# Performance work log

Hardware: AMD Instinct MI355X
Metric: run time of the kernel (lower is better)

## Reference

```python
import jax, jax.numpy as jnp
import numpy as np

B, S, D, V = 2, 4096, 2048, 32000
H, HD = 16, 128          # heads, head dim (H*HD == D)
BS = 16                  # block_size
N_ANCH = 128             # num_anchors (static: loss_mask=ones guarantees enough valid positions)
MASK_ID = 31999
DFF = 8192


def rms(x, w, eps=1e-6):
    return x * jax.lax.rsqrt(jnp.mean(x * x, axis=-1, keepdims=True) + eps) * w


def rope(x, pos):
    # x: (..., L, H, hd), pos: (..., L)
    hd = x.shape[-1]
    inv = 1.0 / (10000.0 ** (jnp.arange(0, hd, 2, dtype=jnp.float32) / hd))
    ang = pos[..., None, None].astype(jnp.float32) * inv  # (..., L, 1, hd/2)
    cos, sin = jnp.cos(ang), jnp.sin(ang)
    x1, x2 = x[..., : hd // 2], x[..., hd // 2 :]
    return jnp.concatenate([x1 * cos - x2 * sin, x2 * cos + x1 * sin], axis=-1).astype(x.dtype)


def setup_inputs() -> dict:
    key = jax.random.key(0)
    ks = jax.random.split(key, 12)
    s = 0.02
    return {
        "input_ids": jax.random.randint(ks[0], (B, S), 0, V, dtype=jnp.int32),
        "hidden_states": jax.random.normal(ks[1], (B, S, D), dtype=jnp.float32),
        "loss_mask": jnp.ones((B, S), dtype=jnp.float32),
        "rand_vals": jax.random.uniform(ks[2], (B, S - BS + 1), dtype=jnp.float32),
        "embed_table": jax.random.normal(ks[3], (V, D), dtype=jnp.float32) * s,
        "lm_head_w": jax.random.normal(ks[4], (V, D), dtype=jnp.float32) * s,
        "wq": jax.random.normal(ks[5], (D, D), dtype=jnp.float32) * s,
        "wk": jax.random.normal(ks[6], (D, D), dtype=jnp.float32) * s,
        "wv": jax.random.normal(ks[7], (D, D), dtype=jnp.float32) * s,
        "wo": jax.random.normal(ks[8], (D, D), dtype=jnp.float32) * s,
        "w_gate": jax.random.normal(ks[9], (D, DFF), dtype=jnp.float32) * s,
        "w_up": jax.random.normal(ks[10], (D, DFF), dtype=jnp.float32) * s,
        "w_down": jax.random.normal(ks[11], (DFF, D), dtype=jnp.float32) * s,
        "norm_attn": jnp.ones((D,), dtype=jnp.float32),
        "norm_mlp": jnp.ones((D,), dtype=jnp.float32),
        "norm_out": jnp.ones((D,), dtype=jnp.float32),
        "norm_chs": jnp.ones((D,), dtype=jnp.float32),
    }


def reference(input_ids, hidden_states, loss_mask, rand_vals, embed_table, lm_head_w,
              wq, wk, wv, wo, w_gate, w_up, w_down, norm_attn, norm_mlp, norm_out, norm_chs):
    max_anchor = S - BS
    # ---- anchor sampling: random permutation of valid positions via argsort of rand ----
    valid = loss_mask[:, : max_anchor + 1] > 0.5                       # (B, max_anchor+1)
    valid_counts = valid.sum(axis=1)
    idx = jnp.arange(max_anchor + 1, dtype=jnp.int32)
    masked_idx = jnp.where(valid, idx[None, :], S + 1)
    rv = jnp.where(valid, rand_vals, 2.0)
    order = jnp.argsort(rv, axis=1)
    gathered = jnp.take_along_axis(masked_idx, order, axis=1)
    anchors = jnp.sort(gathered[:, :N_ANCH], axis=1)                   # (B, N)
    keep = jnp.arange(N_ANCH)[None, :] < jnp.minimum(valid_counts, N_ANCH)[:, None]
    anchors = jnp.where(keep, anchors, 0)
    # ---- noise embedding: anchor token at block start, mask token elsewhere ----
    anchor_tok = jnp.take_along_axis(input_ids, jnp.clip(anchors, 0, S - 1), axis=1)
    first_tok = jnp.where(keep, anchor_tok, MASK_ID)
    noise_ids = jnp.full((B, N_ANCH, BS), MASK_ID, dtype=jnp.int32).at[:, :, 0].set(first_tok)
    x = embed_table[noise_ids]                                         # (B,N,BS,D)
    # ---- CHS context hidden: target hidden at anchor-1 ----
    ctx_pos = jnp.maximum(anchors - 1, 0)
    ctx = jnp.take_along_axis(hidden_states, ctx_pos[:, :, None], axis=1)  # (B,N,D)
    # ---- block-diagonal attention: per-block kv = [CHS_i | draft block i] (kv_len=1+BS) ----
    pos_q = anchors[:, :, None] + jnp.arange(BS)[None, None, :]        # (B,N,BS)
    pos_kv = jnp.concatenate([ctx_pos[:, :, None], pos_q], axis=2)     # (B,N,1+BS)
    hq = rms(x, norm_attn)
    hc = rms(ctx, norm_chs)[:, :, None, :]
    kv_in = jnp.concatenate([hc, hq], axis=2)                          # (B,N,1+BS,D)
    q = rope((hq @ wq).reshape(B, N_ANCH, BS, H, HD), pos_q)
    k = rope((kv_in @ wk).reshape(B, N_ANCH, 1 + BS, H, HD), pos_kv)
    v = (kv_in @ wv).reshape(B, N_ANCH, 1 + BS, H, HD)
    scores = jnp.einsum('bnqhd,bnkhd->bnhqk', q, k) * (1.0 / HD ** 0.5)
    attn = jax.nn.softmax(scores, axis=-1)
    out = jnp.einsum('bnhqk,bnkhd->bnqhd', attn, v).reshape(B, N_ANCH, BS, D) @ wo
    out = out * keep[:, :, None, None].astype(out.dtype)               # invalid blocks fully masked
    x = x + out
    h = rms(x, norm_mlp)
    x = x + (jax.nn.silu(h @ w_gate) * (h @ w_up)) @ w_down
    h_out = rms(x, norm_out)
    logits = h_out @ lm_head_w.T                                       # (B,N,BS,V)
    # ---- block-wise CE loss ----
    label_idx = anchors[:, :, None] + jnp.arange(BS)[None, None, :]
    valid_label = label_idx < S
    safe = jnp.minimum(label_idx, S - 1)
    targets = jnp.take_along_axis(jnp.broadcast_to(input_ids[:, None, :], (B, N_ANCH, S)), safe, axis=2)
    lm_g = jnp.take_along_axis(jnp.broadcast_to(loss_mask[:, None, :], (B, N_ANCH, S)), safe, axis=2)
    weight = (keep[:, :, None] & valid_label).astype(jnp.float32)
    weight = weight * (jnp.arange(BS) > 0)[None, None, :].astype(jnp.float32) * lm_g
    logp = jax.nn.log_softmax(logits, axis=-1)
    tok_logp = jnp.take_along_axis(logp, targets[..., None].astype(jnp.int32), axis=-1)[..., 0]
    loss = -(tok_logp * weight).sum() / (weight.sum() + 1e-6)
    pred = jnp.argmax(logits, axis=-1)
    accuracy = ((pred == targets) & (weight > 0.5)).sum().astype(jnp.float32) / (weight.sum() + 1e-6)
    return loss, accuracy
```

## Files before the change

### kernel.cpp

```cpp
#include <hip/hip_runtime.h>
#include <math.h>

typedef unsigned short u16;
typedef short v8s __attribute__((ext_vector_type(8)));
typedef u16   v4u __attribute__((ext_vector_type(4)));
typedef float v4f __attribute__((ext_vector_type(4)));

#define DEVFN static __device__ __forceinline__

constexpr int cB = 2, cS = 4096, cD = 2048, cV = 32000, cH = 16, cHD = 128;
constexpr int cBS = 16, cNA = 128, cMASK = 31999, cDFF = 8192;
constexpr int NCAND = cS - cBS + 1;
constexpr int MTOK  = cB * cNA * cBS;
constexpr int MKV   = cB * cNA * 17;
constexpr int NCH   = cV / 128;
constexpr int NCH2  = cV / 256;

constexpr int EPI_BF16 = 0, EPI_SILU = 1, EPI_OEMB = 2, EPI_DOWNACC = 3, EPI_STATS = 4;
constexpr int ASRC_BF16 = 0, ASRC_RMS = 1, ASRC_AOMAP = 2;

struct RmsSrc {
  const float* hs; const float* emb; const float* nattn; const float* nchs;
  const float* rowinv; const int* ftok; const int* cpos;
};

DEVFN u16 f2bf(float f) {
  union { float f; unsigned u; } a; a.f = f;
  unsigned u = a.u;
  u = u + 0x7fffu + ((u >> 16) & 1u);
  return (u16)(u >> 16);
}
DEVFN float bf2f(u16 h) {
  union { unsigned u; float f; } a; a.u = ((unsigned)h) << 16;
  return a.f;
}
DEVFN float waveSum(float v) {
  #pragma unroll
  for (int o = 32; o >= 1; o >>= 1) v += __shfl_xor(v, o);
  return v;
}
DEVFN void gload16(void* lds, const void* g) {
  __builtin_amdgcn_global_load_lds(
      (const __attribute__((address_space(1))) unsigned*)g,
      (__attribute__((address_space(3))) unsigned*)lds, 16, 0, 0);
}

__global__ void k_select(const float* __restrict__ lmask, const float* __restrict__ rv_in,
                         int* __restrict__ self) {
  int b = blockIdx.x >> 4, chunk = blockIdx.x & 15;
  __shared__ float rvs[4096];
  for (int i = threadIdx.x; i < NCAND; i += 256) {
    bool valid = lmask[(size_t)b * cS + i] > 0.5f;
    rvs[i] = valid ? rv_in[(size_t)b * NCAND + i] : 2.0f;
  }
  __syncthreads();
  int i = chunk * 256 + threadIdx.x;
  if (i < NCAND) {
    float v = rvs[i];
    int rank = 0;
    for (int j = 0; j < NCAND; ++j) {
      float u = rvs[j];
      rank += (u < v) || (u == v && j < i);
    }
    self[(size_t)b * NCAND + i] = (rank < cNA) ? 1 : 0;
  }
}

__global__ void k_anchors(const float* __restrict__ lmask, const int* __restrict__ self,
                          const int* __restrict__ ids, int* __restrict__ anchors,
                          int* __restrict__ keepA, int* __restrict__ ftok, int* __restrict__ cpos) {
  int b = blockIdx.x;
  __shared__ int flags[4096];
  __shared__ int ssum[256];
  __shared__ int soff[257];
  __shared__ int abuf[cNA];
  for (int i = threadIdx.x; i < 4096; i += 256)
    flags[i] = (i < NCAND) ? (self[(size_t)b * NCAND + i] && (lmask[(size_t)b * cS + i] > 0.5f)) : 0;
  if (threadIdx.x < cNA) abuf[threadIdx.x] = 0;
  __syncthreads();
  int s = 0;
  #pragma unroll
  for (int j = 0; j < 16; ++j) s += flags[threadIdx.x * 16 + j];
  ssum[threadIdx.x] = s;
  __syncthreads();
  if (threadIdx.x == 0) {
    int a = 0;
    for (int t = 0; t < 256; ++t) { soff[t] = a; a += ssum[t]; }
    soff[256] = a;
  }
  __syncthreads();
  int nsel = soff[256];
  int p = soff[threadIdx.x];
  for (int j = 0; j < 16; ++j) {
    int i = threadIdx.x * 16 + j;
    if (flags[i]) { if (p < cNA) abuf[p] = i; ++p; }
  }
  __syncthreads();
// ... 19 lines not shown
                              : emb + (size_t)((j == 1) ? ftok[bn] : cMASK) * cD;
  float ss = 0.f;
  for (int d = threadIdx.x; d < cD; d += 256) { float v = src[d]; ss += v * v; }
  ss = waveSum(ss);
  __shared__ float red[4];
  if ((threadIdx.x & 63) == 0) red[threadIdx.x >> 6] = ss;
  __syncthreads();
  if (threadIdx.x == 0) {
    float tot = red[0] + red[1] + red[2] + red[3];
    rowinv[r] = 1.0f / sqrtf(tot / cD + 1e-6f);
  }
}

__global__ void k_build2(const float* __restrict__ hs, const float* __restrict__ emb,
                         const float* __restrict__ nattn, const float* __restrict__ nchs,
                         const int* __restrict__ ftok, const int* __restrict__ cpos,
                         u16* __restrict__ kv) {
  int r = blockIdx.x;
  int j = r % 17, bn = r / 17, b = bn >> 7;
  const float* src; const float* w;
  if (j == 0) { src = hs + ((size_t)b * cS + cpos[bn]) * cD; w = nchs; }
  else {
    int tok = (j == 1) ? ftok[bn] : cMASK;
    src = emb + (size_t)tok * cD; w = nattn;
  }
  float ss = 0.f;
  for (int d = threadIdx.x; d < cD; d += 256) { float v = src[d]; ss += v * v; }
  ss = waveSum(ss);
  __shared__ float red[4];
  if ((threadIdx.x & 63) == 0) red[threadIdx.x >> 6] = ss;
  __syncthreads();
  float tot = red[0] + red[1] + red[2] + red[3];
  float inv = 1.0f / sqrtf(tot / cD + 1e-6f);
  for (int d = threadIdx.x; d < cD; d += 256)
    kv[(size_t)r * cD + d] = f2bf(src[d] * inv * w[d]);
}

__global__ void k_rms(const float* __restrict__ xin, const float* __restrict__ w,
                      u16* __restrict__ outp) {
  int m = blockIdx.x;
  const float* row = xin + (size_t)m * cD;
  float ss = 0.f;
  for (int d = threadIdx.x; d < cD; d += 256) { float v = row[d]; ss += v * v; }
  ss = waveSum(ss);
  __shared__ float red[4];
  if ((threadIdx.x & 63) == 0) red[threadIdx.x >> 6] = ss;
  __syncthreads();
  float tot = red[0] + red[1] + red[2] + red[3];
  float inv = 1.0f / sqrtf(tot / cD + 1e-6f);
  for (int d = threadIdx.x; d < cD; d += 256)
    outp[(size_t)m * cD + d] = f2bf(row[d] * inv * w[d]);
}

__global__ void k_conv(const float* __restrict__ in, u16* __restrict__ out, long n) {
  long i = ((long)blockIdx.x * 256 + threadIdx.x) * 8;
  long stride = (long)gridDim.x * 256 * 8;
  for (; i < n; i += stride) {
    v4f a = *(const v4f*)(in + i), b = *(const v4f*)(in + i + 4);
    v8s pk;
    #pragma unroll
    for (int e = 0; e < 4; ++e) { pk[e] = (short)f2bf(a[e]); pk[4 + e] = (short)f2bf(b[e]); }
    *(v8s*)(out + i) = pk;
  }
}

__global__ void k_tconv(const float* __restrict__ W, u16* __restrict__ WT, int K, int N) {
  __shared__ u16 t[64][72];
  int n0 = blockIdx.x * 64, k0 = blockIdx.y * 64;
  int tid = threadIdx.x;
  int c4 = (tid & 15) * 4, r0 = tid >> 4;
  #pragma unroll
  for (int rr = 0; rr < 64; rr += 16) {
    int k = r0 + rr;
    v4f v = *(const v4f*)(W + (size_t)(k0 + k) * N + n0 + c4);
    #pragma unroll
    for (int e = 0; e < 4; ++e) t[c4 + e][k] = f2bf(v[e]);
  }
  __syncthreads();
  int n = tid >> 2, kq = (tid & 3) * 16;
  v8s o0, o1;
  #pragma unroll
  for (int e = 0; e < 8; ++e) { o0[e] = (short)t[n][kq + e]; o1[e] = (short)t[n][kq + 8 + e]; }
  *(v8s*)(WT + (size_t)(n0 + n) * K + k0 + kq) = o0;
  *(v8s*)(WT + (size_t)(n0 + n) * K + k0 + kq + 8) = o1;
}

template <int EPI>
__launch_bounds__(512, 2)
__global__ void k_gemm3(const u16* __restrict__ Abf, const u16* __restrict__ Bbf,
                        u16* __restrict__ Cbf, const u16* __restrict__ Gaux,
                        v4f* __restrict__ partials, int K, int ldc, int nch) {
  __shared__ __align__(16) u16 lds[2][32768];
  const int tid = threadIdx.x;
  const int lane = tid & 63, wid = tid >> 6;
  const int wm = wid >> 2, wn = wid & 3;
  const int lc = lane & 15, lq = lane >> 4;
  const int m0 = blockIdx.x * 256, n0 = blockIdx.y * 256;

  const u16* srcA[4]; const u16* srcB[4];
  #pragma unroll
  for (int i = 0; i < 4; ++i) {
    int s = i * 512 + tid;
    int row = s >> 3;
    int c3 = (s & 7) ^ (row & 7);
    srcA[i] = Abf + (size_t)(m0 + row) * K + c3 * 8;
    srcB[i] = Bbf + (size_t)(n0 + row) * K + c3 * 8;
  }

  v4f acc[8][4];
  #pragma unroll
  for (int i = 0; i < 8; ++i)
    #pragma unroll
    for (int j = 0; j < 4; ++j) acc[i][j] = (v4f){0.f, 0.f, 0.f, 0.f};

  const int sw = lc & 7;
  const int aoff0 = (((wm * 128 + lc) * 8 + 0 + lq) ^ sw) * 8;
  const int aoff1 = (((wm * 128 + lc) * 8 + 4 + lq) ^ sw) * 8;
  const int boff0 = (((wn * 64 + lc) * 8 + 0 + lq) ^ sw) * 8;
  const int boff1 = (((wn * 64 + lc) * 8 + 4 + lq) ^ sw) * 8;

  auto stageTo = [&](int b) {
    u16* dA = &lds[b][0] + wid * 512;
    u16* dB = &lds[b][16384] + wid * 512;
    #pragma unroll
    for (int i = 0; i < 4; ++i) { gload16(dA + i * 4096, srcA[i]); srcA[i] += 64; }
    #pragma unroll
    for (int i = 0; i < 4; ++i) { gload16(dB + i * 4096, srcB[i]); srcB[i] += 64; }
  };

  stageTo(0);
  const int NT = K >> 6;
  for (int t = 0; t < NT; ++t) {
    const int cur = t & 1;
    if (t + 1 < NT) {
      stageTo(cur ^ 1);
      asm volatile("s_waitcnt vmcnt(8)" ::: "memory");
    } else {
      asm volatile("s_waitcnt vmcnt(0)" ::: "memory");
    }
    __builtin_amdgcn_s_barrier();
    const u16* Ab = &lds[cur][0];
    const u16* Bb = &lds[cur][16384];
    v8s a0[8], a1[8], b0[4], b1[4];
    #pragma unroll
    for (int mi = 0; mi < 8; ++mi) a0[mi] = *(const v8s*)(Ab + aoff0 + mi * 1024);
    #pragma unroll
    for (int ni = 0; ni < 4; ++ni) b0[ni] = *(const v8s*)(Bb + boff0 + ni * 1024);
    #pragma unroll
    for (int mi = 0; mi < 8; ++mi) a1[mi] = *(const v8s*)(Ab + aoff1 + mi * 1024);
    #pragma unroll
    for (int ni = 0; ni < 4; ++ni) b1[ni] = *(const v8s*)(Bb + boff1 + ni * 1024);
    __builtin_amdgcn_s_setprio(1);
    #pragma unroll
    for (int mi = 0; mi < 8; ++mi)
      #pragma unroll
      for (int ni = 0; ni < 4; ++ni)
        acc[mi][ni] = __builtin_amdgcn_mfma_f32_16x16x32_bf16(a0[mi], b0[ni], acc[mi][ni], 0, 0, 0);
    __builtin_amdgcn_s_setprio(0);
    asm volatile("s_waitcnt lgkmcnt(0)" ::: "memory");
    __builtin_amdgcn_sched_barrier(0);
    __builtin_amdgcn_s_barrier();
    __builtin_amdgcn_s_setprio(1);
    #pragma unroll
    for (int mi = 0; mi < 8; ++mi)
      #pragma unroll
      for (int ni = 0; ni < 4; ++ni)
        acc[mi][ni] = __builtin_amdgcn_mfma_f32_16x16x32_bf16(a1[mi], b1[ni], acc[mi][ni], 0, 0, 0);
    __builtin_amdgcn_s_setprio(0);
  }

  if constexpr (EPI == EPI_STATS) {
    __shared__ float s_mx[1024], s_sm[1024];
    __shared__ int   s_ax[1024];
    __syncthreads();
    #pragma unroll
    for (int mi = 0; mi < 8; ++mi) {
      #pragma unroll
      for (int r = 0; r < 4; ++r) {
        float v0 = acc[mi][0][r], v1 = acc[mi][1][r], v2 = acc[mi][2][r], v3 = acc[mi][3][r];
        float mx = v0; int ax = lc;
        if (v1 > mx) { mx = v1; ax = 16 + lc; }
        if (v2 > mx) { mx = v2; ax = 32 + lc; }
        if (v3 > mx) { mx = v3; ax = 48 + lc; }
        #pragma unroll
        for (int off = 1; off < 16; off <<= 1) {
          float om = __shfl_xor(mx, off); int oa = __shfl_xor(ax, off);
          if (om > mx || (om == mx && oa < ax)) { mx = om; ax = oa; }
        }
        float se = __expf(v0 - mx) + __expf(v1 - mx) + __expf(v2 - mx) + __expf(v3 - mx);
        #pragma unroll
        for (int off = 1; off < 16; off <<= 1) se += __shfl_xor(se, off);
        if (lc == 0) {
          int row = wm * 128 + mi * 16 + lq * 4 + r;
          s_mx[row * 4 + wn] = mx; s_sm[row * 4 + wn] = se; s_ax[row * 4 + wn] = wn * 64 + ax;
        }
      }
    }
    __syncthreads();
    if (tid < 256) {
      float gm = s_mx[tid * 4]; int ga = s_ax[tid * 4];
      #pragma unroll
      for (int w = 1; w < 4; ++w) {
        float m = s_mx[tid * 4 + w];
        if (m > gm) { gm = m; ga = s_ax[tid * 4 + w]; }
      }
      float gs = 0.f;
      #pragma unroll
      for (int w = 0; w < 4; ++w) gs += s_sm[tid * 4 + w] * __expf(s_mx[tid * 4 + w] - gm);
      v4f rec; rec[0] = gm; rec[1] = gs; rec[2] = __int_as_float(n0 + ga); rec[3] = 0.f;
      partials[(size_t)(m0 + tid) * nch + blockIdx.y] = rec;
    }
    return;
  } else {
    #pragma unroll
    for (int mi = 0; mi < 8; ++mi)
      #pragma unroll
      for (int ni = 0; ni < 4; ++ni)
        #pragma unroll
        for (int r = 0; r < 4; ++r) {
          int grow = m0 + wm * 128 + mi * 16 + lq * 4 + r;
          int gcol = n0 + wn * 64 + ni * 16 + lc;
          size_t idx = (size_t)grow * ldc + gcol;
          float vv = acc[mi][ni][r];
          if constexpr (EPI == EPI_BF16) {
            Cbf[idx] = f2bf(vv);
          } else {
            float g = bf2f(Gaux[idx]);
            Cbf[idx] = f2bf(vv * g / (1.0f + __expf(-g)));
          }
        }
  }
}

template <int ASRC, int EPI>
__launch_bounds__(256, 2)
__global__ void k_gemm4(const u16* __restrict__ Abf, const u16* __restrict__ Bbf,
                        u16* __restrict__ Cbf, float* __restrict__ Cf32,
                        const int* __restrict__ keepArr, RmsSrc rs, int K, int ldc) {
  __shared__ __align__(16) u16 lds[2][16384];
  const int tid = threadIdx.x;
  const int lane = tid & 63, wid = tid >> 6;
  const int wm = wid >> 1, wn = wid & 1;
  const int lc = lane & 15, lq = lane >> 4;
  const int m0 = blockIdx.x * 128, n0 = blockIdx.y * 128;

  const u16* srcA[4]; const u16* srcB[4];
  #pragma unroll
  for (int i = 0; i < 4; ++i) {
    int s = i * 256 + tid;
    int row = s >> 3;
    int c3 = (s & 7) ^ (row & 7);
    int ar = m0 + row;
    if constexpr (ASRC == ASRC_AOMAP) ar = (ar >> 4) * 17 + 1 + (ar & 15);
    srcA[i] = Abf + (size_t)ar * K + c3 * 8;
    srcB[i] = Bbf + (size_t)(n0 + row) * K + c3 * 8;
  }

  v4f acc[4][4];
  #pragma unroll
  for (int i = 0; i < 4; ++i)
    #pragma unroll
    for (int j = 0; j < 4; ++j) acc[i][j] = (v4f){0.f, 0.f, 0.f, 0.f};

  const int sw = lc & 7;
  const int aoff0 = (((wm * 64 + lc) * 8 + 0 + lq) ^ sw) * 8;
  const int aoff1 = (((wm * 64 + lc) * 8 + 4 + lq) ^ sw) * 8;
  const int boff0 = (((wn * 64 + lc) * 8 + 0 + lq) ^ sw) * 8;
  const int boff1 = (((wn * 64 + lc) * 8 + 4 + lq) ^ sw) * 8;

  auto stageTo = [&](int b) {
    u16* dA = &lds[b][0] + wid * 512;
    u16* dB = &lds[b][8192] + wid * 512;
    #pragma unroll
    for (int i = 0; i < 4; ++i) { gload16(dA + i * 2048, srcA[i]); srcA[i] += 64; }
    #pragma unroll
    for (int i = 0; i < 4; ++i) { gload16(dB + i * 2048, srcB[i]); srcB[i] += 64; }
  };

  stageTo(0);
  const int NT = K >> 6;
  for (int t = 0; t < NT; ++t) {
    const int cur = t & 1;
    if (t + 1 < NT) {
      stageTo(cur ^ 1);
      asm volatile("s_waitcnt vmcnt(8)" ::: "memory");
    } else {
      asm volatile("s_waitcnt vmcnt(0)" ::: "memory");
    }
    __builtin_amdgcn_s_barrier();
    const u16* Ab = &lds[cur][0];
    const u16* Bb = &lds[cur][8192];
    v8s a0[4], a1[4], b0[4], b1[4];
    #pragma unroll
    for (int mi = 0; mi < 4; ++mi) a0[mi] = *(const v8s*)(Ab + aoff0 + mi * 1024);
    #pragma unroll
    for (int ni = 0; ni < 4; ++ni) b0[ni] = *(const v8s*)(Bb + boff0 + ni * 1024);
    #pragma unroll
    for (int mi = 0; mi < 4; ++mi) a1[mi] = *(const v8s*)(Ab + aoff1 + mi * 1024);
    #pragma unroll
    for (int ni = 0; ni < 4; ++ni) b1[ni] = *(const v8s*)(Bb + boff1 + ni * 1024);
    __builtin_amdgcn_s_setprio(1);
    #pragma unroll
    for (int mi = 0; mi < 4; ++mi)
      #pragma unroll
      for (int ni = 0; ni < 4; ++ni)
        acc[mi][ni] = __builtin_amdgcn_mfma_f32_16x16x32_bf16(a0[mi], b0[ni], acc[mi][ni], 0, 0, 0);
    __builtin_amdgcn_s_setprio(0);
    asm volatile("s_waitcnt lgkmcnt(0)" ::: "memory");
// ... 355 lines not shown
  const float* wd    = (const float*)d_in[12];
  const float* nattn = (const float*)d_in[13];
  const float* nmlp  = (const float*)d_in[14];
  const float* nout  = (const float*)d_in[15];
  const float* nchs  = (const float*)d_in[16];
  (void)in_sizes; (void)n_in; (void)out_size;

  float* outp = (float*)d_out;
  k_heartbeat<<<dim3(1), 64, 0, stream>>>(outp);

  char* wsb = (char*)d_ws;
  size_t off = 0;
  auto alloc = [&](size_t bytes) -> void* {
    void* p = wsb + off;
    off = (off + bytes + 255) & ~(size_t)255;
    return p;
  };
  int*   anchors = (int*)  alloc((size_t)cB * cNA * 4);
  int*   keepA   = (int*)  alloc((size_t)cB * cNA * 4);
  int*   ftok    = (int*)  alloc((size_t)cB * cNA * 4);
  int*   cpos    = (int*)  alloc((size_t)cB * cNA * 4);
  int*   self    = (int*)  alloc((size_t)cB * NCAND * 4);
  float* rowinv  = (float*)alloc((size_t)MKV * 4);
  int*   ttok    = (int*)  alloc((size_t)MTOK * 4);
  float* tlogit  = (float*)alloc((size_t)MTOK * 4);
  float* tokOut  = (float*)alloc((size_t)MTOK * 4 * 4);

  const size_t szQ  = (size_t)MKV * cD * 2;
  const size_t szX  = (size_t)MTOK * cD * 4;
  u16* qb = (u16*)alloc(szQ);
  const size_t a1off = off;

  RmsSrc rs{hs, emb, nattn, nchs, rowinv, ftok, cpos};

  k_select <<<dim3(cB * 16), 256, 0, stream>>>(lmask, rv, self);
  k_anchors<<<dim3(cB),      256, 0, stream>>>(lmask, self, ids, anchors, keepA, ftok, cpos);

  const size_t szKV   = szQ;
  const size_t szCbuf = (size_t)MTOK * 4096 * 2;
  size_t kvb_off  = a1off;
  size_t a1f_off  = (kvb_off + szKV + 255) & ~(size_t)255;
  size_t a1f_sz   = 2 * szQ > (szX + szCbuf) ? 2 * szQ : (szX + szCbuf);
  size_t wreg_off = (a1f_off + a1f_sz + 255) & ~(size_t)255;
  size_t wreg_sz  = (size_t)cV * cD * 2;
  size_t need_fast = wreg_off + wreg_sz;

  if (need_fast <= ws_size) {
    u16*   kvb   = (u16*)(wsb + kvb_off);
    u16*   kb    = (u16*)(wsb + a1f_off);
    u16*   vb    = (u16*)(wsb + a1f_off + szQ);
    float* xb    = (float*)(wsb + a1f_off);
    u16*   cbuf  = (u16*)(wsb + a1f_off + szX);
    v4f*   parts = (v4f*)(wsb + a1f_off);
    u16*   hb    = qb;
    u16*   houtb = qb;
    u16*   wT    = (u16*)(wsb + wreg_off);
    const size_t szDD = (size_t)cD * cD;
    u16* wqT = wT;            u16* wkT = wT + szDD;
    u16* wvT = wT + 2 * szDD; u16* woT = wT + 3 * szDD;
    const size_t szDF = (size_t)cD * cDFF;
    u16* wgT = wT; u16* wuT = wT + szDF; u16* wdT = wT + 2 * szDF;
    u16* wlmT = wT;

    k_build2<<<dim3(MKV), 256, 0, stream>>>(hs, emb, nattn, nchs, ftok, cpos, kvb);

    k_tconv<<<dim3(32, 32), 256, 0, stream>>>(wq, wqT, cD, cD);
    k_tconv<<<dim3(32, 32), 256, 0, stream>>>(wk, wkT, cD, cD);
    k_tconv<<<dim3(32, 32), 256, 0, stream>>>(wv, wvT, cD, cD);
    k_tconv<<<dim3(32, 32), 256, 0, stream>>>(wo, woT, cD, cD);

    k_gemm4<ASRC_BF16, EPI_BF16><<<dim3(MKV / 128, cD / 128), 256, 0, stream>>>(
        kvb, wqT, qb, nullptr, nullptr, rs, cD, cD);
    k_gemm4<ASRC_BF16, EPI_BF16><<<dim3(MKV / 128, cD / 128), 256, 0, stream>>>(
        kvb, wkT, kb, nullptr, nullptr, rs, cD, cD);
    k_gemm4<ASRC_BF16, EPI_BF16><<<dim3(MKV / 128, cD / 128), 256, 0, stream>>>(
        kvb, wvT, vb, nullptr, nullptr, rs, cD, cD);

    k_rope<<<dim3(2 * MKV), 256, 0, stream>>>(qb, kb, anchors, cpos);
    k_attn<<<dim3(cB * cNA * cH), 64, 0, stream>>>(qb, kb, vb);

    k_gemm4<ASRC_AOMAP, EPI_OEMB><<<dim3(MTOK / 128, cD / 128), 256, 0, stream>>>(
        qb, woT, nullptr, xb, keepA, rs, cD, cD);

    k_rms<<<dim3(MTOK), 256, 0, stream>>>(xb, nmlp, hb);

    k_tconv<<<dim3(128, 32), 256, 0, stream>>>(wg, wgT, cD, cDFF);
    k_tconv<<<dim3(128, 32), 256, 0, stream>>>(wu, wuT, cD, cDFF);
    k_tconv<<<dim3(32, 128), 256, 0, stream>>>(wd, wdT, cDFF, cD);

    for (int cb = 0; cb < cDFF; cb += 4096) {
      k_gemm3<EPI_BF16><<<dim3(MTOK / 256, 16), 512, 0, stream>>>(
          hb, wgT + (size_t)cb * cD, cbuf, nullptr, nullptr, cD, 4096, 0);
      k_gemm3<EPI_SILU><<<dim3(MTOK / 256, 16), 512, 0, stream>>>(
          hb, wuT + (size_t)cb * cD, cbuf, cbuf, nullptr, cD, 4096, 0);
      k_gemm4<ASRC_BF16, EPI_DOWNACC><<<dim3(MTOK / 128, cD / 128), 256, 0, stream>>>(
          cbuf, wdT + cb, nullptr, xb, nullptr, rs, 4096, cD);
    }

    k_rms<<<dim3(MTOK), 256, 0, stream>>>(xb, nout, houtb);

    k_tgt<<<dim3(MTOK / 4), 256, 0, stream>>>(houtb, wlm, ids, anchors, ttok, tlogit);

    k_conv<<<dim3(2048), 256, 0, stream>>>(wlm, wlmT, (long)cV * cD);
    k_gemm3<EPI_STATS><<<dim3(MTOK / 256, NCH2), 512, 0, stream>>>(
        houtb, wlmT, nullptr, nullptr, parts, cD, 0, NCH2);

    k_combine<<<dim3(MTOK), 256, 0, stream>>>(parts, ttok, tlogit, keepA, anchors, lmask, tokOut, NCH2);
    k_final  <<<dim3(1), 256, 0, stream>>>(tokOut, outp);
    return;
  }

  const int cwopts[4] = {4096, 2048, 1024, 512};
  int CW = 0;
  for (int ci = 0; ci < 4; ++ci) {
    int cw = cwopts[ci];
    size_t cbufsz = (size_t)MTOK * cw * 2;
    size_t s1 = 2 * szQ;
    size_t s2 = szX + cbufsz;
    size_t sz = s1 > s2 ? s1 : s2;
    size_t pmin = (size_t)MTOK * NCH * 16;
    if (pmin > sz) sz = pmin;
    if (a1off + sz <= ws_size) { CW = cw; break; }
  }
  if (CW == 0) { k_sentinel<<<dim3(1), 64, 0, stream>>>(outp); return; }

  u16*   kb    = (u16*)(wsb + a1off);
  u16*   vb    = (u16*)(wsb + a1off + szQ);
  float* xb    = (float*)(wsb + a1off);
  u16*   cbuf  = (u16*)(wsb + a1off + szX);
  v4f*   parts = (v4f*)(wsb + a1off);
  u16*   hb    = qb;
  u16*   houtb = qb;

  k_rowinv<<<dim3(MKV), 256, 0, stream>>>(hs, emb, ftok, cpos, rowinv);

  k_gemm<ASRC_RMS, 0, EPI_BF16><<<dim3(MKV / 128, cD / 128), 256, 0, stream>>>(
      nullptr, wq, qb, nullptr, nullptr, nullptr, nullptr, rs, cD, cD, cD);
  k_gemm<ASRC_RMS, 0, EPI_BF16><<<dim3(MKV / 128, cD / 128), 256, 0, stream>>>(
      nullptr, wk, kb, nullptr, nullptr, nullptr, nullptr, rs, cD, cD, cD);
  k_gemm<ASRC_RMS, 0, EPI_BF16><<<dim3(MKV / 128, cD / 128), 256, 0, stream>>>(
      nullptr, wv, vb, nullptr, nullptr, nullptr, nullptr, rs, cD, cD, cD);

  k_rope<<<dim3(2 * MKV), 256, 0, stream>>>(qb, kb, anchors, cpos);
  k_attn<<<dim3(cB * cNA * cH), 64, 0, stream>>>(qb, kb, vb);

  k_gemm<ASRC_AOMAP, 0, EPI_OEMB><<<dim3(MTOK / 128, cD / 128), 256, 0, stream>>>(
      qb, wo, nullptr, xb, nullptr, keepA, nullptr, rs, cD, cD, cD);

  k_rms<<<dim3(MTOK), 256, 0, stream>>>(xb, nmlp, hb);

  for (int cb = 0; cb < cDFF; cb += CW) {
    k_gemm<ASRC_BF16, 0, EPI_BF16><<<dim3(MTOK / 128, CW / 128), 256, 0, stream>>>(
        hb, wg + cb, cbuf, nullptr, nullptr, nullptr, nullptr, rs, cD, cDFF, CW);
    k_gemm<ASRC_BF16, 0, EPI_SILU><<<dim3(MTOK / 128, CW / 128), 256, 0, stream>>>(
        hb, wu + cb, cbuf, nullptr, cbuf, nullptr, nullptr, rs, cD, cDFF, CW);
    k_gemm<ASRC_BF16, 0, EPI_DOWNACC><<<dim3(MTOK / 128, cD / 128), 256, 0, stream>>>(
        cbuf, wd + (size_t)cb * cD, nullptr, xb, nullptr, nullptr, nullptr, rs, CW, cD, cD);
  }
// ... 11 lines not shown
```

Measured before the change: 1.691 ms.

## Run LM-head stats GEMM in FP8 with scaled weights and FP8 activations

```diff
diff --git a/kernel.cpp b/kernel.cpp
--- a/kernel.cpp
+++ b/kernel.cpp
@@ -2,9 +2,11 @@
 #include <math.h>
 
 typedef unsigned short u16;
+typedef unsigned char u8;
 typedef short v8s __attribute__((ext_vector_type(8)));
 typedef u16   v4u __attribute__((ext_vector_type(4)));
 typedef float v4f __attribute__((ext_vector_type(4)));
+typedef int   v2i __attribute__((ext_vector_type(2)));
 
 #define DEVFN static __device__ __forceinline__
 
@@ -43,6 +45,11 @@
   __builtin_amdgcn_global_load_lds(
       (const __attribute__((address_space(1))) unsigned*)g,
       (__attribute__((address_space(3))) unsigned*)lds, 16, 0, 0);
+}
+DEVFN int pack4fp8(float a, float b, float c, float d) {
+  int p = __builtin_amdgcn_cvt_pk_fp8_f32(a, b, 0, 0);
+  p = __builtin_amdgcn_cvt_pk_fp8_f32(c, d, p, 1);
+  return p;
 }
 
 __global__ void k_select(const float* __restrict__ lmask, const float* __restrict__ rv_in,
@@ -168,15 +175,27 @@
     outp[(size_t)m * cD + d] = f2bf(row[d] * inv * w[d]);
 }
 
-__global__ void k_conv(const float* __restrict__ in, u16* __restrict__ out, long n) {
+__global__ void k_conv8(const float* __restrict__ in, u8* __restrict__ out, long n, float scale) {
   long i = ((long)blockIdx.x * 256 + threadIdx.x) * 8;
   long stride = (long)gridDim.x * 256 * 8;
   for (; i < n; i += stride) {
     v4f a = *(const v4f*)(in + i), b = *(const v4f*)(in + i + 4);
-    v8s pk;
-    #pragma unroll
-    for (int e = 0; e < 4; ++e) { pk[e] = (short)f2bf(a[e]); pk[4 + e] = (short)f2bf(b[e]); }
-    *(v8s*)(out + i) = pk;
+    v2i pk;
+    pk[0] = pack4fp8(a[0] * scale, a[1] * scale, a[2] * scale, a[3] * scale);
+    pk[1] = pack4fp8(b[0] * scale, b[1] * scale, b[2] * scale, b[3] * scale);
+    *(v2i*)(out + i) = pk;
+  }
+}
+
+__global__ void k_cvt8(const u16* __restrict__ in, u8* __restrict__ out, long n) {
+  long i = ((long)blockIdx.x * 256 + threadIdx.x) * 8;
+  long stride = (long)gridDim.x * 256 * 8;
+  for (; i < n; i += stride) {
+    v8s a = *(const v8s*)(in + i);
+    v2i pk;
+    pk[0] = pack4fp8(bf2f((u16)a[0]), bf2f((u16)a[1]), bf2f((u16)a[2]), bf2f((u16)a[3]));
+    pk[1] = pack4fp8(bf2f((u16)a[4]), bf2f((u16)a[5]), bf2f((u16)a[6]), bf2f((u16)a[7]));
+    *(v2i*)(out + i) = pk;
   }
 }
 
@@ -285,66 +304,171 @@
     __builtin_amdgcn_s_setprio(0);
   }
 
-  if constexpr (EPI == EPI_STATS) {
-    __shared__ float s_mx[1024], s_sm[1024];
-    __shared__ int   s_ax[1024];
-    __syncthreads();
-    #pragma unroll
-    for (int mi = 0; mi < 8; ++mi) {
+  #pragma unroll
+  for (int mi = 0; mi < 8; ++mi)
+    #pragma unroll
+    for (int ni = 0; ni < 4; ++ni)
       #pragma unroll
       for (int r = 0; r < 4; ++r) {
-        float v0 = acc[mi][0][r], v1 = acc[mi][1][r], v2 = acc[mi][2][r], v3 = acc[mi][3][r];
-        float mx = v0; int ax = lc;
-        if (v1 > mx) { mx = v1; ax = 16 + lc; }
-        if (v2 > mx) { mx = v2; ax = 32 + lc; }
-        if (v3 > mx) { mx = v3; ax = 48 + lc; }
-        #pragma unroll
-        for (int off = 1; off < 16; off <<= 1) {
-          float om = __shfl_xor(mx, off); int oa = __shfl_xor(ax, off);
-          if (om > mx || (om == mx && oa < ax)) { mx = om; ax = oa; }
-        }
-        float se = __expf(v0 - mx) + __expf(v1 - mx) + __expf(v2 - mx) + __expf(v3 - mx);
-        #pragma unroll
-        for (int off = 1; off < 16; off <<= 1) se += __shfl_xor(se, off);
-        if (lc == 0) {
-          int row = wm * 128 + mi * 16 + lq * 4 + r;
-          s_mx[row * 4 + wn] = mx; s_sm[row * 4 + wn] = se; s_ax[row * 4 + wn] = wn * 64 + ax;
+        int grow = m0 + wm * 128 + mi * 16 + lq * 4 + r;
+        int gcol = n0 + wn * 64 + ni * 16 + lc;
+        size_t idx = (size_t)grow * ldc + gcol;
+        float vv = acc[mi][ni][r];
+        if constexpr (EPI == EPI_BF16) {
+          Cbf[idx] = f2bf(vv);
+        } else {
+          float g = bf2f(Gaux[idx]);
+          Cbf[idx] = f2bf(vv * g / (1.0f + __expf(-g)));
         }
       }
-    }
-    __syncthreads();
-    if (tid < 256) {
-      float gm = s_mx[tid * 4]; int ga = s_ax[tid * 4];
-      #pragma unroll
-      for (int w = 1; w < 4; ++w) {
-        float m = s_mx[tid * 4 + w];
-        if (m > gm) { gm = m; ga = s_ax[tid * 4 + w]; }
+  (void)partials; (void)nch;
+}
+
+__launch_bounds__(512, 2)
+__global__ void k_gemm5(const u8* __restrict__ A8, const u8* __restrict__ B8,
+                        v4f* __restrict__ partials, int K, int nch) {
+  __shared__ __align__(16) u8 lds8[2][32768];
+  const int tid = threadIdx.x;
+  const int lane = tid & 63, wid = tid >> 6;
+  const int wm = wid >> 2, wn = wid & 3;
+  const int lc = lane & 15, lq = lane >> 4;
+  const int m0 = blockIdx.x * 256, n0 = blockIdx.y * 256;
+
+  const u8* srcA[2]; const u8* srcB[2];
+  #pragma unroll
+  for (int i = 0; i < 2; ++i) {
+    int s = i * 512 + tid;
+    int row = s >> 2;
+    int fr = (row ^ (row >> 2)) & 3;
+    int c = (s & 3) ^ fr;
+    srcA[i] = A8 + (size_t)(m0 + row) * K + c * 16;
+    srcB[i] = B8 + (size_t)(n0 + row) * K + c * 16;
+  }
+
+  v4f acc[8][4];
+  #pragma unroll
+  for (int i = 0; i < 8; ++i)
+    #pragma unroll
+    for (int j = 0; j < 4; ++j) acc[i][j] = (v4f){0.f, 0.f, 0.f, 0.f};
+
+  int aoffs[8][2];
+  #pragma unroll
+  for (int mi = 0; mi < 8; ++mi) {
+    int row = wm * 128 + mi * 16 + lc;
+    int fr = (row ^ (row >> 2)) & 3;
+    #pragma unroll
+    for (int ks = 0; ks < 2; ++ks) {
+      int slot = ks * 2 + (lq >> 1);
+      aoffs[mi][ks] = row * 64 + ((slot ^ fr) << 4) + ((lq & 1) << 3);
+    }
+  }
+  int boffs[4][2];
+  #pragma unroll
+  for (int ni = 0; ni < 4; ++ni) {
+    int row = wn * 64 + ni * 16 + lc;
+    int fr = (row ^ (row >> 2)) & 3;
+    #pragma unroll
+    for (int ks = 0; ks < 2; ++ks) {
+      int slot = ks * 2 + (lq >> 1);
+      boffs[ni][ks] = row * 64 + ((slot ^ fr) << 4) + ((lq & 1) << 3);
+    }
+  }
+
+  auto stageTo = [&](int b) {
+    u8* dA = &lds8[b][0] + wid * 1024;
+    u8* dB = &lds8[b][16384] + wid * 1024;
+    #pragma unroll
+    for (int i = 0; i < 2; ++i) { gload16(dA + i * 8192, srcA[i]); srcA[i] += 64; }
+    #pragma unroll
+    for (int i = 0; i < 2; ++i) { gload16(dB + i * 8192, srcB[i]); srcB[i] += 64; }
+  };
+
+  stageTo(0);
+  const int NT = K >> 6;
+  for (int t = 0; t < NT; ++t) {
+    const int cur = t & 1;
+    if (t + 1 < NT) {
+      stageTo(cur ^ 1);
+      asm volatile("s_waitcnt vmcnt(4)" ::: "memory");
+    } else {
+      asm volatile("s_waitcnt vmcnt(0)" ::: "memory");
+    }
+    __builtin_amdgcn_s_barrier();
+    const u8* Ab = &lds8[cur][0];
+    const u8* Bb = &lds8[cur][16384];
+    long long a0[8], a1[8], b0[4], b1[4];
+    #pragma unroll
+    for (int mi = 0; mi < 8; ++mi) a0[mi] = *(const long long*)(Ab + aoffs[mi][0]);
+    #pragma unroll
+    for (int ni = 0; ni < 4; ++ni) b0[ni] = *(const long long*)(Bb + boffs[ni][0]);
+    #pragma unroll
+    for (int mi = 0; mi < 8; ++mi) a1[mi] = *(const long long*)(Ab + aoffs[mi][1]);
+    #pragma unroll
+    for (int ni = 0; ni < 4; ++ni) b1[ni] = *(const long long*)(Bb + boffs[ni][1]);
+    __builtin_amdgcn_s_setprio(1);
+    #pragma unroll
+    for (int mi = 0; mi < 8; ++mi)
+      #pragma unroll
+      for (int ni = 0; ni < 4; ++ni)
+        acc[mi][ni] = __builtin_amdgcn_mfma_f32_16x16x32_fp8_fp8(a0[mi], b0[ni], acc[mi][ni], 0, 0, 0);
+    __builtin_amdgcn_s_setprio(0);
+    asm volatile("s_waitcnt lgkmcnt(0)" ::: "memory");
+    __builtin_amdgcn_sched_barrier(0);
+    __builtin_amdgcn_s_barrier();
+    __builtin_amdgcn_s_setprio(1);
+    #pragma unroll
+    for (int mi = 0; mi < 8; ++mi)
+      #pragma unroll
+      for (int ni = 0; ni < 4; ++ni)
+        acc[mi][ni] = __builtin_amdgcn_mfma_f32_16x16x32_fp8_fp8(a1[mi], b1[ni], acc[mi][ni], 0, 0, 0);
+    __builtin_amdgcn_s_setprio(0);
+  }
+
+  #pragma unroll
+  for (int mi = 0; mi < 8; ++mi)
+    #pragma unroll
+    for (int ni = 0; ni < 4; ++ni)
+      acc[mi][ni] *= 0.015625f;
+
+  __shared__ float s_mx[1024], s_sm[1024];
+  __shared__ int   s_ax[1024];
+  __syncthreads();
+  #pragma unroll
+  for (int mi = 0; mi < 8; ++mi) {
+    #pragma unroll
+    for (int r = 0; r < 4; ++r) {
+      float v0 = acc[mi][0][r], v1 = acc[mi][1][r], v2 = acc[mi][2][r], v3 = acc[mi][3][r];
+      float mx = v0; int ax = lc;
+      if (v1 > mx) { mx = v1; ax = 16 + lc; }
+      if (v2 > mx) { mx = v2; ax = 32 + lc; }
+      if (v3 > mx) { mx = v3; ax = 48 + lc; }
+      #pragma unroll
+      for (int off = 1; off < 16; off <<= 1) {
+        float om = __shfl_xor(mx, off); int oa = __shfl_xor(ax, off);
+        if (om > mx || (om == mx && oa < ax)) { mx = om; ax = oa; }
       }
-      float gs = 0.f;
-      #pragma unroll
-      for (int w = 0; w < 4; ++w) gs += s_sm[tid * 4 + w] * __expf(s_mx[tid * 4 + w] - gm);
-      v4f rec; rec[0] = gm; rec[1] = gs; rec[2] = __int_as_float(n0 + ga); rec[3] = 0.f;
-      partials[(size_t)(m0 + tid) * nch + blockIdx.y] = rec;
-    }
-    return;
-  } else {
-    #pragma unroll
-    for (int mi = 0; mi < 8; ++mi)
-      #pragma unroll
-      for (int ni = 0; ni < 4; ++ni)
-        #pragma unroll
-        for (int r = 0; r < 4; ++r) {
-          int grow = m0 + wm * 128 + mi * 16 + lq * 4 + r;
-          int gcol = n0 + wn * 64 + ni * 16 + lc;
-          size_t idx = (size_t)grow * ldc + gcol;
-          float vv = acc[mi][ni][r];
-          if constexpr (EPI == EPI_BF16) {
-            Cbf[idx] = f2bf(vv);
-          } else {
-            float g = bf2f(Gaux[idx]);
-            Cbf[idx] = f2bf(vv * g / (1.0f + __expf(-g)));
-          }
-        }
+      float se = __expf(v0 - mx) + __expf(v1 - mx) + __expf(v2 - mx) + __expf(v3 - mx);
+      #pragma unroll
+      for (int off = 1; off < 16; off <<= 1) se += __shfl_xor(se, off);
+      if (lc == 0) {
+        int row = wm * 128 + mi * 16 + lq * 4 + r;
+        s_mx[row * 4 + wn] = mx; s_sm[row * 4 + wn] = se; s_ax[row * 4 + wn] = wn * 64 + ax;
+      }
+    }
+  }
+  __syncthreads();
+  if (tid < 256) {
+    float gm = s_mx[tid * 4]; int ga = s_ax[tid * 4];
+    #pragma unroll
+    for (int w = 1; w < 4; ++w) {
+      float m = s_mx[tid * 4 + w];
+      if (m > gm) { gm = m; ga = s_ax[tid * 4 + w]; }
+    }
+    float gs = 0.f;
+    #pragma unroll
+    for (int w = 0; w < 4; ++w) gs += s_sm[tid * 4 + w] * __expf(s_mx[tid * 4 + w] - gm);
+    v4f rec; rec[0] = gm; rec[1] = gs; rec[2] = __int_as_float(n0 + ga); rec[3] = 0.f;
+    partials[(size_t)(m0 + tid) * nch + blockIdx.y] = rec;
   }
 }
 
@@ -352,7 +476,7 @@
 __launch_bounds__(256, 2)
 __global__ void k_gemm4(const u16* __restrict__ Abf, const u16* __restrict__ Bbf,
                         u16* __restrict__ Cbf, float* __restrict__ Cf32,
-                        const int* __restrict__ keepArr, RmsSrc rs, int K, int ldc) {
+                        const int* __restrict__ keepArr, RmsSrc rs, int K, int ldb, int ldc) {
   __shared__ __align__(16) u16 lds[2][16384];
   const int tid = threadIdx.x;
   const int lane = tid & 63, wid = tid >> 6;
@@ -369,7 +493,7 @@
     int ar = m0 + row;
     if constexpr (ASRC == ASRC_AOMAP) ar = (ar >> 4) * 17 + 1 + (ar & 15);
     srcA[i] = Abf + (size_t)ar * K + c3 * 8;
-    srcB[i] = Bbf + (size_t)(n0 + row) * K + c3 * 8;
+    srcB[i] = Bbf + (size_t)(n0 + row) * ldb + c3 * 8;
   }
 
   v4f acc[4][4];
@@ -831,6 +955,7 @@
     float* xb    = (float*)(wsb + a1f_off);
     u16*   cbuf  = (u16*)(wsb + a1f_off + szX);
     v4f*   parts = (v4f*)(wsb + a1f_off);
+    u8*    h8    = (u8*)(wsb + a1f_off + (size_t)16 * 1024 * 1024);
     u16*   hb    = qb;
     u16*   houtb = qb;
     u16*   wT    = (u16*)(wsb + wreg_off);
@@ -839,7 +964,7 @@
     u16* wvT = wT + 2 * szDD; u16* woT = wT + 3 * szDD;
     const size_t szDF = (size_t)cD * cDFF;
     u16* wgT = wT; u16* wuT = wT + szDF; u16* wdT = wT + 2 * szDF;
-    u16* wlmT = wT;
+    u8*  wlm8 = (u8*)wT;
 
     k_build2<<<dim3(MKV), 256, 0, stream>>>(hs, emb, nattn, nchs, ftok, cpos, kvb);
 
@@ -849,17 +974,17 @@
     k_tconv<<<dim3(32, 32), 256, 0, stream>>>(wo, woT, cD, cD);
 
     k_gemm4<ASRC_BF16, EPI_BF16><<<dim3(MKV / 128, cD / 128), 256, 0, stream>>>(
-        kvb, wqT, qb, nullptr, nullptr, rs, cD, cD);
+        kvb, wqT, qb, nullptr, nullptr, rs, cD, cD, cD);
     k_gemm4<ASRC_BF16, EPI_BF16><<<dim3(MKV / 128, cD / 128), 256, 0, stream>>>(
-        kvb, wkT, kb, nullptr, nullptr, rs, cD, cD);
+        kvb, wkT, kb, nullptr, nullptr, rs, cD, cD, cD);
     k_gemm4<ASRC_BF16, EPI_BF16><<<dim3(MKV / 128, cD / 128), 256, 0, stream>>>(
-        kvb, wvT, vb, nullptr, nullptr, rs, cD, cD);
+        kvb, wvT, vb, nullptr, nullptr, rs, cD, cD, cD);
 
     k_rope<<<dim3(2 * MKV), 256, 0, stream>>>(qb, kb, anchors, cpos);
     k_attn<<<dim3(cB * cNA * cH), 64, 0, stream>>>(qb, kb, vb);
 
     k_gemm4<ASRC_AOMAP, EPI_OEMB><<<dim3(MTOK / 128, cD / 128), 256, 0, stream>>>(
-        qb, woT, nullptr, xb, keepA, rs, cD, cD);
+        qb, woT, nullptr, xb, keepA, rs, cD, cD, cD);
 
     k_rms<<<dim3(MTOK), 256, 0, stream>>>(xb, nmlp, hb);
 
@@ -873,16 +998,16 @@
       k_gemm3<EPI_SILU><<<dim3(MTOK / 256, 16), 512, 0, stream>>>(
           hb, wuT + (size_t)cb * cD, cbuf, cbuf, nullptr, cD, 4096, 0);
       k_gemm4<ASRC_BF16, EPI_DOWNACC><<<dim3(MTOK / 128, cD / 128), 256, 0, stream>>>(
-          cbuf, wdT + cb, nullptr, xb, nullptr, rs, 4096, cD);
+          cbuf, wdT + cb, nullptr, xb, nullptr, rs, 4096, cDFF, cD);
     }
 
     k_rms<<<dim3(MTOK), 256, 0, stream>>>(xb, nout, houtb);
 
     k_tgt<<<dim3(MTOK / 4), 256, 0, stream>>>(houtb, wlm, ids, anchors, ttok, tlogit);
 
-    k_conv<<<dim3(2048), 256, 0, stream>>>(wlm, wlmT, (long)cV * cD);
-    k_gemm3<EPI_STATS><<<dim3(MTOK / 256, NCH2), 512, 0, stream>>>(
-        houtb, wlmT, nullptr, nullptr, parts, cD, 0, NCH2);
+    k_cvt8 <<<dim3(1024), 256, 0, stream>>>(houtb, h8, (long)MTOK * cD);
+    k_conv8<<<dim3(2048), 256, 0, stream>>>(wlm, wlm8, (long)cV * cD, 64.0f);
+    k_gemm5<<<dim3(MTOK / 256, NCH2), 512, 0, stream>>>(h8, wlm8, parts, cD, NCH2);
 
     k_combine<<<dim3(MTOK), 256, 0, stream>>>(parts, ttok, tlogit, keepA, anchors, lmask, tokOut, NCH2);
     k_final  <<<dim3(1), 256, 0, stream>>>(tokOut, outp);
```

New measurement: 1.629 ms. 3.7% less time.

## Replace 256x256 GEMM with k-half-split LDS pipeline and fix down-proj B stride

Applied to the files above, without the earlier changes.

```diff
diff --git a/kernel.cpp b/kernel.cpp
--- a/kernel.cpp
+++ b/kernel.cpp
@@ -202,25 +202,25 @@
 }
 
 template <int EPI>
-__launch_bounds__(512, 2)
-__global__ void k_gemm3(const u16* __restrict__ Abf, const u16* __restrict__ Bbf,
+__launch_bounds__(512, 1)
+__global__ void k_gemm6(const u16* __restrict__ Abf, const u16* __restrict__ Bbf,
                         u16* __restrict__ Cbf, const u16* __restrict__ Gaux,
                         v4f* __restrict__ partials, int K, int ldc, int nch) {
-  __shared__ __align__(16) u16 lds[2][32768];
+  __shared__ __align__(16) u16 lds[65536];
   const int tid = threadIdx.x;
   const int lane = tid & 63, wid = tid >> 6;
   const int wm = wid >> 2, wn = wid & 3;
   const int lc = lane & 15, lq = lane >> 4;
   const int m0 = blockIdx.x * 256, n0 = blockIdx.y * 256;
 
-  const u16* srcA[4]; const u16* srcB[4];
-  #pragma unroll
-  for (int i = 0; i < 4; ++i) {
+  const u16* srcA[2]; const u16* srcB[2];
+  #pragma unroll
+  for (int i = 0; i < 2; ++i) {
     int s = i * 512 + tid;
-    int row = s >> 3;
-    int c3 = (s & 7) ^ (row & 7);
-    srcA[i] = Abf + (size_t)(m0 + row) * K + c3 * 8;
-    srcB[i] = Bbf + (size_t)(n0 + row) * K + c3 * 8;
+    int row = s >> 2;
+    int c2 = (s & 3) ^ ((row >> 1) & 3);
+    srcA[i] = Abf + (size_t)(m0 + row) * K + c2 * 8;
+    srcB[i] = Bbf + (size_t)(n0 + row) * K + c2 * 8;
   }
 
   v4f acc[8][4];
@@ -229,61 +229,106 @@
     #pragma unroll
     for (int j = 0; j < 4; ++j) acc[i][j] = (v4f){0.f, 0.f, 0.f, 0.f};
 
-  const int sw = lc & 7;
-  const int aoff0 = (((wm * 128 + lc) * 8 + 0 + lq) ^ sw) * 8;
-  const int aoff1 = (((wm * 128 + lc) * 8 + 4 + lq) ^ sw) * 8;
-  const int boff0 = (((wn * 64 + lc) * 8 + 0 + lq) ^ sw) * 8;
-  const int boff1 = (((wn * 64 + lc) * 8 + 4 + lq) ^ sw) * 8;
-
-  auto stageTo = [&](int b) {
-    u16* dA = &lds[b][0] + wid * 512;
-    u16* dB = &lds[b][16384] + wid * 512;
-    #pragma unroll
-    for (int i = 0; i < 4; ++i) { gload16(dA + i * 4096, srcA[i]); srcA[i] += 64; }
-    #pragma unroll
-    for (int i = 0; i < 4; ++i) { gload16(dB + i * 4096, srcB[i]); srcB[i] += 64; }
+  const int fsw = lq ^ ((lc >> 1) & 3);
+  int aoff[8], boff[4];
+  #pragma unroll
+  for (int mi = 0; mi < 8; ++mi) aoff[mi] = ((wm * 128 + mi * 16 + lc) * 4 + fsw) * 8;
+  #pragma unroll
+  for (int ni = 0; ni < 4; ++ni) boff[ni] = ((wn * 64 + ni * 16 + lc) * 4 + fsw) * 8;
+
+  auto stageA = [&](int t, int kh) {
+    int reg = (t & 1) * 32768 + kh * 8192;
+    int koff = t * 64 + kh * 32;
+    #pragma unroll
+    for (int i = 0; i < 2; ++i)
+      gload16(&lds[reg + i * 4096 + wid * 512], srcA[i] + koff);
   };
-
-  stageTo(0);
+  auto stageB = [&](int t, int kh) {
+    int reg = (t & 1) * 32768 + 16384 + kh * 8192;
+    int koff = t * 64 + kh * 32;
+    #pragma unroll
+    for (int i = 0; i < 2; ++i)
+      gload16(&lds[reg + i * 4096 + wid * 512], srcB[i] + koff);
+  };
+
+  stageA(0, 0); stageB(0, 0);
+  stageA(0, 1); stageB(0, 1);
+  stageA(1, 0); stageB(1, 0);
+  asm volatile("s_waitcnt vmcnt(8)" ::: "memory");
+  __builtin_amdgcn_s_barrier();
+
   const int NT = K >> 6;
   for (int t = 0; t < NT; ++t) {
-    const int cur = t & 1;
-    if (t + 1 < NT) {
-      stageTo(cur ^ 1);
-      asm volatile("s_waitcnt vmcnt(8)" ::: "memory");
-    } else {
-      asm volatile("s_waitcnt vmcnt(0)" ::: "memory");
-    }
-    __builtin_amdgcn_s_barrier();
-    const u16* Ab = &lds[cur][0];
-    const u16* Bb = &lds[cur][16384];
-    v8s a0[8], a1[8], b0[4], b1[4];
-    #pragma unroll
-    for (int mi = 0; mi < 8; ++mi) a0[mi] = *(const v8s*)(Ab + aoff0 + mi * 1024);
-    #pragma unroll
-    for (int ni = 0; ni < 4; ++ni) b0[ni] = *(const v8s*)(Bb + boff0 + ni * 1024);
-    #pragma unroll
-    for (int mi = 0; mi < 8; ++mi) a1[mi] = *(const v8s*)(Ab + aoff1 + mi * 1024);
-    #pragma unroll
-    for (int ni = 0; ni < 4; ++ni) b1[ni] = *(const v8s*)(Bb + boff1 + ni * 1024);
-    __builtin_amdgcn_s_setprio(1);
-    #pragma unroll
-    for (int mi = 0; mi < 8; ++mi)
-      #pragma unroll
-      for (int ni = 0; ni < 4; ++ni)
-        acc[mi][ni] = __builtin_amdgcn_mfma_f32_16x16x32_bf16(a0[mi], b0[ni], acc[mi][ni], 0, 0, 0);
-    __builtin_amdgcn_s_setprio(0);
+    const int bufb = (t & 1) * 32768;
+    const u16* Ab0 = &lds[bufb];
+    const u16* Ab1 = &lds[bufb + 8192];
+    const u16* Bb0 = &lds[bufb + 16384];
+    const u16* Bb1 = &lds[bufb + 24576];
+    v8s a_[4], b_[4];
+
+    #pragma unroll
+    for (int ni = 0; ni < 4; ++ni) b_[ni] = *(const v8s*)(Bb0 + boff[ni]);
+    #pragma unroll
+    for (int mi = 0; mi < 4; ++mi) a_[mi] = *(const v8s*)(Ab0 + aoff[mi]);
+    if (t + 1 < NT) stageA(t + 1, 1);
     asm volatile("s_waitcnt lgkmcnt(0)" ::: "memory");
     __builtin_amdgcn_sched_barrier(0);
+    __builtin_amdgcn_s_setprio(1);
+    #pragma unroll
+    for (int mi = 0; mi < 4; ++mi)
+      #pragma unroll
+      for (int ni = 0; ni < 4; ++ni)
+        acc[mi][ni] = __builtin_amdgcn_mfma_f32_16x16x32_bf16(a_[mi], b_[ni], acc[mi][ni], 0, 0, 0);
+    __builtin_amdgcn_s_setprio(0);
     __builtin_amdgcn_s_barrier();
+
+    #pragma unroll
+    for (int mi = 0; mi < 4; ++mi) a_[mi] = *(const v8s*)(Ab0 + aoff[mi + 4]);
+    if (t + 1 < NT) stageB(t + 1, 1);
+    asm volatile("s_waitcnt lgkmcnt(0)" ::: "memory");
+    __builtin_amdgcn_sched_barrier(0);
     __builtin_amdgcn_s_setprio(1);
     #pragma unroll
-    for (int mi = 0; mi < 8; ++mi)
+    for (int mi = 0; mi < 4; ++mi)
       #pragma unroll
       for (int ni = 0; ni < 4; ++ni)
-        acc[mi][ni] = __builtin_amdgcn_mfma_f32_16x16x32_bf16(a1[mi], b1[ni], acc[mi][ni], 0, 0, 0);
+        acc[mi + 4][ni] = __builtin_amdgcn_mfma_f32_16x16x32_bf16(a_[mi], b_[ni], acc[mi + 4][ni], 0, 0, 0);
     __builtin_amdgcn_s_setprio(0);
-  }
+    if (t + 1 < NT) { asm volatile("s_waitcnt vmcnt(4)" ::: "memory"); }
+    else            { asm volatile("s_waitcnt vmcnt(0)" ::: "memory"); }
+    __builtin_amdgcn_s_barrier();
+
+    #pragma unroll
+    for (int ni = 0; ni < 4; ++ni) b_[ni] = *(const v8s*)(Bb1 + boff[ni]);
+    #pragma unroll
+    for (int mi = 0; mi < 4; ++mi) a_[mi] = *(const v8s*)(Ab1 + aoff[mi]);
+    if (t + 2 < NT) stageA(t + 2, 0);
+    asm volatile("s_waitcnt lgkmcnt(0)" ::: "memory");
+    __builtin_amdgcn_sched_barrier(0);
+    __builtin_amdgcn_s_setprio(1);
+    #pragma unroll
+    for (int mi = 0; mi < 4; ++mi)
+      #pragma unroll
+      for (int ni = 0; ni < 4; ++ni)
+        acc[mi][ni] = __builtin_amdgcn_mfma_f32_16x16x32_bf16(a_[mi], b_[ni], acc[mi][ni], 0, 0, 0);
+    __builtin_amdgcn_s_setprio(0);
+    __builtin_amdgcn_s_barrier();
+
+    #pragma unroll
+    for (int mi = 0; mi < 4; ++mi) a_[mi] = *(const v8s*)(Ab1 + aoff[mi + 4]);
+    if (t + 2 < NT) stageB(t + 2, 0);
+    asm volatile("s_waitcnt lgkmcnt(0)" ::: "memory");
+    __builtin_amdgcn_sched_barrier(0);
+    __builtin_amdgcn_s_setprio(1);
+    #pragma unroll
+    for (int mi = 0; mi < 4; ++mi)
+      #pragma unroll
+      for (int ni = 0; ni < 4; ++ni)
+        acc[mi + 4][ni] = __builtin_amdgcn_mfma_f32_16x16x32_bf16(a_[mi], b_[ni], acc[mi + 4][ni], 0, 0, 0);
+    __builtin_amdgcn_s_setprio(0);
+    __builtin_amdgcn_s_barrier();
+  }
+  asm volatile("s_waitcnt vmcnt(0)" ::: "memory");
 
   if constexpr (EPI == EPI_STATS) {
     __shared__ float s_mx[1024], s_sm[1024];
@@ -352,7 +397,7 @@
 __launch_bounds__(256, 2)
 __global__ void k_gemm4(const u16* __restrict__ Abf, const u16* __restrict__ Bbf,
                         u16* __restrict__ Cbf, float* __restrict__ Cf32,
-                        const int* __restrict__ keepArr, RmsSrc rs, int K, int ldc) {
+                        const int* __restrict__ keepArr, RmsSrc rs, int K, int ldb, int ldc) {
   __shared__ __align__(16) u16 lds[2][16384];
   const int tid = threadIdx.x;
   const int lane = tid & 63, wid = tid >> 6;
@@ -369,7 +414,7 @@
     int ar = m0 + row;
     if constexpr (ASRC == ASRC_AOMAP) ar = (ar >> 4) * 17 + 1 + (ar & 15);
     srcA[i] = Abf + (size_t)ar * K + c3 * 8;
-    srcB[i] = Bbf + (size_t)(n0 + row) * K + c3 * 8;
+    srcB[i] = Bbf + (size_t)(n0 + row) * ldb + c3 * 8;
   }
 
   v4f acc[4][4];
@@ -849,17 +894,17 @@
     k_tconv<<<dim3(32, 32), 256, 0, stream>>>(wo, woT, cD, cD);
 
     k_gemm4<ASRC_BF16, EPI_BF16><<<dim3(MKV / 128, cD / 128), 256, 0, stream>>>(
-        kvb, wqT, qb, nullptr, nullptr, rs, cD, cD);
+        kvb, wqT, qb, nullptr, nullptr, rs, cD, cD, cD);
     k_gemm4<ASRC_BF16, EPI_BF16><<<dim3(MKV / 128, cD / 128), 256, 0, stream>>>(
-        kvb, wkT, kb, nullptr, nullptr, rs, cD, cD);
+        kvb, wkT, kb, nullptr, nullptr, rs, cD, cD, cD);
     k_gemm4<ASRC_BF16, EPI_BF16><<<dim3(MKV / 128, cD / 128), 256, 0, stream>>>(
-        kvb, wvT, vb, nullptr, nullptr, rs, cD, cD);
+        kvb, wvT, vb, nullptr, nullptr, rs, cD, cD, cD);
 
     k_rope<<<dim3(2 * MKV), 256, 0, stream>>>(qb, kb, anchors, cpos);
     k_attn<<<dim3(cB * cNA * cH), 64, 0, stream>>>(qb, kb, vb);
 
     k_gemm4<ASRC_AOMAP, EPI_OEMB><<<dim3(MTOK / 128, cD / 128), 256, 0, stream>>>(
-        qb, woT, nullptr, xb, keepA, rs, cD, cD);
+        qb, woT, nullptr, xb, keepA, rs, cD, cD, cD);
 
     k_rms<<<dim3(MTOK), 256, 0, stream>>>(xb, nmlp, hb);
 
@@ -868,12 +913,12 @@
     k_tconv<<<dim3(32, 128), 256, 0, stream>>>(wd, wdT, cDFF, cD);
 
     for (int cb = 0; cb < cDFF; cb += 4096) {
-      k_gemm3<EPI_BF16><<<dim3(MTOK / 256, 16), 512, 0, stream>>>(
+      k_gemm6<EPI_BF16><<<dim3(MTOK / 256, 16), 512, 0, stream>>>(
           hb, wgT + (size_t)cb * cD, cbuf, nullptr, nullptr, cD, 4096, 0);
-      k_gemm3<EPI_SILU><<<dim3(MTOK / 256, 16), 512, 0, stream>>>(
+      k_gemm6<EPI_SILU><<<dim3(MTOK / 256, 16), 512, 0, stream>>>(
           hb, wuT + (size_t)cb * cD, cbuf, cbuf, nullptr, cD, 4096, 0);
       k_gemm4<ASRC_BF16, EPI_DOWNACC><<<dim3(MTOK / 128, cD / 128), 256, 0, stream>>>(
-          cbuf, wdT + cb, nullptr, xb, nullptr, rs, 4096, cD);
+          cbuf, wdT + cb, nullptr, xb, nullptr, rs, 4096, cDFF, cD);
     }
 
     k_rms<<<dim3(MTOK), 256, 0, stream>>>(xb, nout, houtb);
@@ -881,7 +926,7 @@
     k_tgt<<<dim3(MTOK / 4), 256, 0, stream>>>(houtb, wlm, ids, anchors, ttok, tlogit);
 
     k_conv<<<dim3(2048), 256, 0, stream>>>(wlm, wlmT, (long)cV * cD);
-    k_gemm3<EPI_STATS><<<dim3(MTOK / 256, NCH2), 512, 0, stream>>>(
+    k_gemm6<EPI_STATS><<<dim3(MTOK / 256, NCH2), 512, 0, stream>>>(
         houtb, wlmT, nullptr, nullptr, parts, cD, 0, NCH2);
 
     k_combine<<<dim3(MTOK), 256, 0, stream>>>(parts, ttok, tlogit, keepA, anchors, lmask, tokOut, NCH2);
```

After: 1.657 ms. 2.0% less time.
